# Kernel optimization log

Hardware: AMD Instinct MI355X
Metric: run time of the kernel (lower is better)

## Reference

```python
import jax, jax.numpy as jnp
import numpy as np

B, H, W, C = 8, 28, 28, 1024
NH = 16
HD = C // NH          # head dim 64
HID = 4 * C           # mlp hidden 4096
BC = C // 2           # bottleneck channels 512
SCALE = HD ** -0.5


def setup_inputs() -> dict:
    key = jax.random.key(0)
    ks = iter(jax.random.split(key, 32))
    def rn(shape, s=0.02):
        return jax.random.normal(next(ks), shape, jnp.float32) * s
    return dict(
        x=jax.random.normal(next(ks), (B, H, W, C), jnp.float32),
        norm1_w=jnp.ones((C,), jnp.float32), norm1_b=jnp.zeros((C,), jnp.float32),
        qkv_w=rn((C, 3 * C)), qkv_b=jnp.zeros((3 * C,), jnp.float32),
        proj_w=rn((C, C)), proj_b=jnp.zeros((C,), jnp.float32),
        rel_h=rn((2 * H - 1, HD)), rel_w=rn((2 * W - 1, HD)),
        norm2_w=jnp.ones((C,), jnp.float32), norm2_b=jnp.zeros((C,), jnp.float32),
        fc1_w=rn((C, HID)), fc1_b=jnp.zeros((HID,), jnp.float32),
        fc2_w=rn((HID, C)), fc2_b=jnp.zeros((C,), jnp.float32),
        conv1_w=rn((1, 1, C, BC)), ln1_w=jnp.ones((BC,), jnp.float32), ln1_b=jnp.zeros((BC,), jnp.float32),
        conv2_w=rn((3, 3, BC, BC)), ln2_w=jnp.ones((BC,), jnp.float32), ln2_b=jnp.zeros((BC,), jnp.float32),
        conv3_w=rn((1, 1, BC, C)), ln3_w=rn((C,)), ln3_b=rn((C,)),
    )


def _ln(x, w, b, eps):
    # layernorm over last axis (channels in NHWC)
    m = jnp.mean(x, -1, keepdims=True)
    v = jnp.mean((x - m) ** 2, -1, keepdims=True)
    return (x - m) * jax.lax.rsqrt(v + eps) * w + b


def _conv(x, w, pad):
    return jax.lax.conv_general_dilated(
        x, w, (1, 1), pad, dimension_numbers=('NHWC', 'HWIO', 'NHWC'))


def _gelu(x):
    return jax.nn.gelu(x, approximate=False)


def _block_forward(x, norm1_w, norm1_b, qkv_w, qkv_b, proj_w, proj_b,
                   rel_h, rel_w, norm2_w, norm2_b, fc1_w, fc1_b, fc2_w, fc2_b,
                   conv1_w, ln1_w, ln1_b, conv2_w, ln2_w, ln2_b, conv3_w, ln3_w, ln3_b):
    S = H * W
    shortcut = x
    xn = _ln(x, norm1_w, norm1_b, 1e-5)

    # ---- attention with decomposed relative position bias ----
    qkv = xn.reshape(B, S, C) @ qkv_w + qkv_b                 # [B,S,3C]
    qkv = qkv.reshape(B, S, 3, NH, HD).transpose(2, 0, 3, 1, 4)  # [3,B,nh,S,hd]
    q, k, v = qkv[0], qkv[1], qkv[2]
    attn = jnp.einsum('bnsd,bntd->bnst', q * SCALE, k)        # [B,nh,S,S]

    idx_h = jnp.arange(H)[:, None] - jnp.arange(H)[None, :] + (H - 1)
    idx_w = jnp.arange(W)[:, None] - jnp.arange(W)[None, :] + (W - 1)
    Rh = rel_h[idx_h]   # [H,H,hd]
    Rw = rel_w[idx_w]   # [W,W,hd]
    qr = q.reshape(B, NH, H, W, HD)
    bias_h = jnp.einsum('bnhwd,hkd->bnhwk', qr, Rh)           # [B,nh,H,W,H]
    bias_w = jnp.einsum('bnhwd,wkd->bnhwk', qr, Rw)           # [B,nh,H,W,W]
    attn = (attn.reshape(B, NH, H, W, H, W)
            + bias_h[..., :, None] + bias_w[..., None, :]).reshape(B, NH, S, S)

    attn = jax.nn.softmax(attn, axis=-1)
    out = jnp.einsum('bnst,bntd->bnsd', attn, v)              # [B,nh,S,hd]
    out = out.transpose(0, 2, 1, 3).reshape(B, H, W, C)
    out = out @ proj_w + proj_b

    x = shortcut + out

    # ---- MLP ----
    xn = _ln(x, norm2_w, norm2_b, 1e-5)
    x = x + (_gelu(xn.reshape(B, S, C) @ fc1_w + fc1_b) @ fc2_w + fc2_b).reshape(B, H, W, C)

    # ---- residual bottleneck conv (channel LayerNorm, eps=1e-6) ----
    out = _conv(x, conv1_w, 'VALID')
    out = _gelu(_ln(out, ln1_w, ln1_b, 1e-6))
    out = _conv(out, conv2_w, ((1, 1), (1, 1)))
    out = _gelu(_ln(out, ln2_w, ln2_b, 1e-6))
    out = _conv(out, conv3_w, 'VALID')
    out = _ln(out, ln3_w, ln3_b, 1e-6)
    return x + out


def reference(x, norm1_w, norm1_b, qkv_w, qkv_b, proj_w, proj_b,
              rel_h, rel_w, norm2_w, norm2_b, fc1_w, fc1_b, fc2_w, fc2_b,
              conv1_w, ln1_w, ln1_b, conv2_w, ln2_w, ln2_b, conv3_w, ln3_w, ln3_b):
    return _block_forward(x, norm1_w, norm1_b, qkv_w, qkv_b, proj_w, proj_b,
                          rel_h, rel_w, norm2_w, norm2_b, fc1_w, fc1_b, fc2_w, fc2_b,
                          conv1_w, ln1_w, ln1_b, conv2_w, ln2_w, ln2_b, conv3_w, ln3_w, ln3_b)
```

## Files before the change

kernel.cpp:

```cpp
#include <hip/hip_runtime.h>
#include <cstdint>
#include <cstddef>

using u16 = unsigned short;
using u32 = unsigned int;

__device__ __forceinline__ float bf2f(u16 u){
  union { u32 i; float f; } x; x.i = ((u32)u) << 16; return x.f;
}
__device__ __forceinline__ u16 f2bf(float f){
  union { float f; u32 i; } x; x.f = f;
  u32 r = x.i + 0x7fffu + ((x.i >> 16) & 1u);
  return (u16)(r >> 16);
}
__device__ __forceinline__ float gelu_f(float x){
  return 0.5f * x * (1.0f + erff(x * 0.70710678118654752f));
}
__device__ __forceinline__ void gld16(const void* g, void* l){
  __builtin_amdgcn_global_load_lds((__attribute__((address_space(1))) void*)(void*)g,
                                   (__attribute__((address_space(3))) void*)l, 16, 0, 0);
}

typedef __bf16 bf16x8 __attribute__((ext_vector_type(8)));
typedef float  f32x4  __attribute__((ext_vector_type(4)));

__global__ __launch_bounds__(256) void k_transpose(const float* __restrict__ src,
                                                   u16* __restrict__ dst, int R, int C){
  __shared__ u16 tile[32][33];
  int bx = blockIdx.x * 32;
  int by = blockIdx.y * 32;
  int tx = threadIdx.x & 31;
  int ty = threadIdx.x >> 5;
  for (int r = ty; r < 32; r += 8)
    tile[r][tx] = f2bf(src[(size_t)(by + r) * C + bx + tx]);
  __syncthreads();
  for (int r = ty; r < 32; r += 8)
    dst[(size_t)(bx + r) * R + by + tx] = tile[tx][r];
}

template<bool IN_F32, bool DO_GELU>
__global__ __launch_bounds__(256) void k_layernorm(const void* __restrict__ inp,
    const float* __restrict__ w, const float* __restrict__ bsh,
    u16* __restrict__ out, int cols, float eps){
  int row = blockIdx.x, t = threadIdx.x;
  size_t base = (size_t)row * cols;
  const float* inf = (const float*)inp;
  const u16*  inb = (const u16*)inp;
  float v[4];
  int ep = cols >> 8;
  float s = 0.f, ss = 0.f;
  for (int e = 0; e < ep; ++e){
    int idx = t + (e << 8);
    float x = IN_F32 ? inf[base + idx] : bf2f(inb[base + idx]);
    v[e] = x; s += x; ss += x * x;
  }
#pragma unroll
  for (int off = 1; off < 64; off <<= 1){
    s  += __shfl_xor(s, off, 64);
    ss += __shfl_xor(ss, off, 64);
  }
  __shared__ float red[8];
  int wv = t >> 6;
  if ((t & 63) == 0){ red[wv] = s; red[4 + wv] = ss; }
  __syncthreads();
  s  = red[0] + red[1] + red[2] + red[3];
  ss = red[4] + red[5] + red[6] + red[7];
  float inv = 1.f / (float)cols;
  float mean = s * inv;
  float var = ss * inv - mean * mean;
  float rs = rsqrtf(var + eps);
  for (int e = 0; e < ep; ++e){
    int idx = t + (e << 8);
    float y = (v[e] - mean) * rs * w[idx] + bsh[idx];
    if (DO_GELU) y = gelu_f(y);
    out[base + idx] = f2bf(y);
  }
}

__global__ __launch_bounds__(256) void k_final(const u16* __restrict__ c3,
    const u16* __restrict__ x2, const float* __restrict__ w,
    const float* __restrict__ bsh, float* __restrict__ out){
  int row = blockIdx.x, t = threadIdx.x;
  size_t base = (size_t)row << 10;
  float v[4];
  float s = 0.f, ss = 0.f;
#pragma unroll
  for (int e = 0; e < 4; ++e){
    int idx = t + (e << 8);
    float x = bf2f(c3[base + idx]);
    v[e] = x; s += x; ss += x * x;
  }
#pragma unroll
  for (int off = 1; off < 64; off <<= 1){
    s  += __shfl_xor(s, off, 64);
    ss += __shfl_xor(ss, off, 64);
  }
  __shared__ float red[8];
  int wv = t >> 6;
  if ((t & 63) == 0){ red[wv] = s; red[4 + wv] = ss; }
  __syncthreads();
  s  = red[0] + red[1] + red[2] + red[3];
  ss = red[4] + red[5] + red[6] + red[7];
  float mean = s * (1.f/1024.f);
  float var = ss * (1.f/1024.f) - mean * mean;
  float rs = rsqrtf(var + 1e-6f);
#pragma unroll
  for (int e = 0; e < 4; ++e){
    int idx = t + (e << 8);
    float y = (v[e] - mean) * rs * w[idx] + bsh[idx];
    out[base + idx] = bf2f(x2[base + idx]) + y;
  }
}

template<bool BIAS, bool GELU, bool RES, bool OUTB, bool OUTF>
__global__ __launch_bounds__(256, 2) void k_gemm(
    const u16* __restrict__ A, const u16* __restrict__ Bt,
    const float* __restrict__ bias, const float* __restrict__ resf,
    u16* __restrict__ outb, float* __restrict__ outf, int N, int K)
{
  __shared__ __align__(16) u16 As[128 * 32];
  __shared__ __align__(16) u16 Bs[128 * 32];
  int t = threadIdx.x, lane = t & 63, wv = t >> 6;
  int m0 = blockIdx.y << 7, n0 = blockIdx.x << 7;
  int wm = (wv >> 1) << 6, wn = (wv & 1) << 6;

  f32x4 acc[4][4];
  const f32x4 z4 = {0.f, 0.f, 0.f, 0.f};
#pragma unroll
  for (int i = 0; i < 4; ++i)
#pragma unroll
    for (int j = 0; j < 4; ++j) acc[i][j] = z4;

  int srow = (wv << 5) + (lane >> 2);
  int skp  = (lane & 3) << 3;
  const u16* Ag = A  + (size_t)(m0 + srow) * K + skp;
  const u16* Bg = Bt + (size_t)(n0 + srow) * K + skp;
  u16* As0 = &As[(wv << 5) * 32];
  u16* As1 = As0 + 16 * 32;
  u16* Bs0 = &Bs[(wv << 5) * 32];
  u16* Bs1 = Bs0 + 16 * 32;
  const size_t rowskip = (size_t)16 * K;

  int fr = lane & 15, fq = (lane >> 4) << 3;

  for (int k0 = 0; k0 < K; k0 += 32){
    gld16(Ag + k0, As0);
    gld16(Ag + rowskip + k0, As1);
    gld16(Bg + k0, Bs0);
    gld16(Bg + rowskip + k0, Bs1);
    __syncthreads();
    bf16x8 af[4], bfr[4];
#pragma unroll
    for (int i = 0; i < 4; ++i)
      af[i] = *(const bf16x8*)&As[(wm + i * 16 + fr) * 32 + fq];
#pragma unroll
    for (int j = 0; j < 4; ++j)
      bfr[j] = *(const bf16x8*)&Bs[(wn + j * 16 + fr) * 32 + fq];
#pragma unroll
    for (int i = 0; i < 4; ++i)
#pragma unroll
      for (int j = 0; j < 4; ++j)
        acc[i][j] = __builtin_amdgcn_mfma_f32_16x16x32_bf16(af[i], bfr[j], acc[i][j], 0, 0, 0);
    __syncthreads();
  }

  int rr = (lane >> 4) << 2;
  int cc = lane & 15;
#pragma unroll
  for (int i = 0; i < 4; ++i)
#pragma unroll
    for (int j = 0; j < 4; ++j){
      int gc = n0 + wn + j * 16 + cc;
      float bb = BIAS ? bias[gc] : 0.f;
#pragma unroll
      for (int r = 0; r < 4; ++r){
        int gr = m0 + wm + i * 16 + rr + r;
        size_t idx = (size_t)gr * N + gc;
        float vv = acc[i][j][r] + bb;
        if (RES) vv += resf[idx];
        if (GELU) vv = gelu_f(vv);
        if (OUTF) outf[idx] = vv;
        if (OUTB) outb[idx] = f2bf(vv);
      }
    }
}

#define ATT_STR 72
__global__ __launch_bounds__(256, 3) void k_attn3(const u16* __restrict__ qkv,
    const float* __restrict__ relh, const float* __restrict__ relw,
    u16* __restrict__ out)
{
  __shared__ __align__(16) u16 k_s[64 * ATT_STR];
  __shared__ __align__(16) u16 vT_s[80 * ATT_STR];
  __shared__ __align__(16) u16 p_s[128 * ATT_STR];
  __shared__ u16 gh_s[128 * 28];
  __shared__ u16 gw_s[128 * 28];

  const int t = threadIdx.x, lane = t & 63, wv = t >> 6;
  int id = blockIdx.x;
  int xr = id & 7, rest = id >> 3;
  int qt = rest % 7, gg = rest / 7;
  int bnh = xr + (gg << 3);
  const int b = bnh >> 4, nh = bnh & 15;
  const int q0 = qt << 7;
  const size_t rowbase = (size_t)b * 784;
  const int wq0 = wv << 5;
  const int fr = lane & 15;
  const int fq = lane >> 4;

  u16* rh_s = p_s;
  u16* rw_s = p_s + 64 * ATT_STR;
  {
    int row = t >> 2, c0 = (t & 3) << 4;
    u16 bh_[16], bw_[16];
    if (row < 55){
      const float* ph = relh + row * 64 + c0;
      const float* pw = relw + row * 64 + c0;
#pragma unroll
      for (int e = 0; e < 16; ++e){ bh_[e] = f2bf(ph[e]); bw_[e] = f2bf(pw[e]); }
    } else {
#pragma unroll
      for (int e = 0; e < 16; ++e){ bh_[e] = 0; bw_[e] = 0; }
    }
    *(uint4*)&rh_s[row * ATT_STR + c0]     = *(uint4*)bh_;
    *(uint4*)&rh_s[row * ATT_STR + c0 + 8] = *(uint4*)(bh_ + 8);
    *(uint4*)&rw_s[row * ATT_STR + c0]     = *(uint4*)bw_;
    *(uint4*)&rw_s[row * ATT_STR + c0 + 8] = *(uint4*)(bw_ + 8);
    for (int idx = t; idx < 16 * ATT_STR; idx += 256){
      int rr = idx / ATT_STR, cc = idx - rr * ATT_STR;
      vT_s[(64 + rr) * ATT_STR + cc] = (rr == 0 && cc < 64) ? (u16)0x3f80 : (u16)0;
    }
  }

  bf16x8 qf[2][2];
#pragma unroll
  for (int mf = 0; mf < 2; ++mf)
#pragma unroll
    for (int ks = 0; ks < 2; ++ks){
      int row = q0 + wq0 + mf * 16 + fr;
      if (row < 784){
        qf[mf][ks] = *(const bf16x8*)(qkv + (rowbase + row) * 3072 + nh * 64 + fq * 8 + ks * 32);
      } else {
        uint4 z = {0u,0u,0u,0u}; qf[mf][ks] = *(bf16x8*)&z;
      }
    }
  __syncthreads();

  const f32x4 z4 = {0.f,0.f,0.f,0.f};
#pragma unroll
  for (int which = 0; which < 2; ++which){
    const u16* rs = which ? rw_s : rh_s;
    f32x4 G[2][4];
#pragma unroll
    for (int mf = 0; mf < 2; ++mf)
#pragma unroll
      for (int nf = 0; nf < 4; ++nf) G[mf][nf] = z4;
#pragma unroll
    for (int nf = 0; nf < 4; ++nf){
      bf16x8 rf0 = *(const bf16x8*)&rs[(nf * 16 + fr) * ATT_STR + fq * 8];
      bf16x8 rf1 = *(const bf16x8*)&rs[(nf * 16 + fr) * ATT_STR + fq * 8 + 32];
#pragma unroll
      for (int mf = 0; mf < 2; ++mf){
        G[mf][nf] = __builtin_amdgcn_mfma_f32_16x16x32_bf16(qf[mf][0], rf0, G[mf][nf], 0, 0, 0);
        G[mf][nf] = __builtin_amdgcn_mfma_f32_16x16x32_bf16(qf[mf][1], rf1, G[mf][nf], 0, 0, 0);
      }
    }
    u16* gt = which ? gw_s : gh_s;
#pragma unroll
    for (int mf = 0; mf < 2; ++mf)
#pragma unroll
      for (int r = 0; r < 4; ++r){
        int lr = wq0 + mf * 16 + fq * 4 + r;
        int grow = q0 + lr;
        int hq = grow / 28;
        int coord = which ? (grow - hq * 28) : hq;
#pragma unroll
        for (int nf = 0; nf < 4; ++nf){
          int j = nf * 16 + fr;
          int kk = coord + 27 - j;
          if ((unsigned)kk < 28u) gt[lr * 28 + kk] = f2bf(G[mf][nf][r]);
        }
      }
  }
  __syncthreads();

  f32x4 acc[2][5];
#pragma unroll
  for (int mf = 0; mf < 2; ++mf)
#pragma unroll
    for (int nf = 0; nf < 5; ++nf) acc[mf][nf] = z4;

  for (int kt = 0; kt < 13; ++kt){
    __syncthreads();
    {
      int krow = lane;
      int d0 = wv << 4;
      int jg = (kt << 6) + krow;
      uint4 kv0 = {0u,0u,0u,0u}, kv1 = {0u,0u,0u,0u};
      uint4 vv0 = {0u,0u,0u,0u}, vv1 = {0u,0u,0u,0u};
      if (jg < 784){
        const u16* kp = qkv + (rowbase + jg) * 3072 + 1024 + nh * 64 + d0;
        kv0 = *(const uint4*)kp; kv1 = *(const uint4*)(kp + 8);
        vv0 = *(const uint4*)(kp + 1024); vv1 = *(const uint4*)(kp + 1032);
      }
      *(uint4*)&k_s[krow * ATT_STR + d0]     = kv0;
      *(uint4*)&k_s[krow * ATT_STR + d0 + 8] = kv1;
      u16 vbuf[16];
      *(uint4*)vbuf = vv0; *(uint4*)(vbuf + 8) = vv1;
#pragma unroll
      for (int e = 0; e < 16; ++e) vT_s[(d0 + e) * ATT_STR + krow] = vbuf[e];
    }
    __syncthreads();

    f32x4 S[2][4];
#pragma unroll
    for (int nf = 0; nf < 4; ++nf){
      bf16x8 kf0 = *(const bf16x8*)&k_s[(nf * 16 + fr) * ATT_STR + fq * 8];
      bf16x8 kf1 = *(const bf16x8*)&k_s[(nf * 16 + fr) * ATT_STR + fq * 8 + 32];
#pragma unroll
      for (int mf = 0; mf < 2; ++mf){
        f32x4 s = z4;
        s = __builtin_amdgcn_mfma_f32_16x16x32_bf16(qf[mf][0], kf0, s, 0, 0, 0);
        s = __builtin_amdgcn_mfma_f32_16x16x32_bf16(qf[mf][1], kf1, s, 0, 0, 0);
        S[mf][nf] = s;
      }
    }

    int hj[4], wj[4]; bool val[4];
#pragma unroll
    for (int nf = 0; nf < 4; ++nf){
      int jg = (kt << 6) + nf * 16 + fr;
      int h = jg / 28;
      hj[nf] = h; wj[nf] = jg - h * 28; val[nf] = (jg < 784);
    }
#pragma unroll
    for (int mf = 0; mf < 2; ++mf)
#pragma unroll
      for (int r = 0; r < 4; ++r){
        int lr = wq0 + mf * 16 + fq * 4 + r;
#pragma unroll
        for (int nf = 0; nf < 4; ++nf){
          float p = 0.f;
          if (val[nf]){
            float bias = bf2f(gh_s[lr * 28 + hj[nf]]) + bf2f(gw_s[lr * 28 + wj[nf]]);
            p = __expf(fmaf(0.125f, S[mf][nf][r], bias));
          }
          p_s[lr * ATT_STR + nf * 16 + fr] = f2bf(p);
        }
      }

#pragma unroll
    for (int ks = 0; ks < 2; ++ks){
      bf16x8 pf0 = *(const bf16x8*)&p_s[(wq0 + fr) * ATT_STR + fq * 8 + ks * 32];
      bf16x8 pf1 = *(const bf16x8*)&p_s[(wq0 + 16 + fr) * ATT_STR + fq * 8 + ks * 32];
#pragma unroll
      for (int nf = 0; nf < 5; ++nf){
        bf16x8 vf = *(const bf16x8*)&vT_s[(nf * 16 + fr) * ATT_STR + fq * 8 + ks * 32];
        acc[0][nf] = __builtin_amdgcn_mfma_f32_16x16x32_bf16(pf0, vf, acc[0][nf], 0, 0, 0);
        acc[1][nf] = __builtin_amdgcn_mfma_f32_16x16x32_bf16(pf1, vf, acc[1][nf], 0, 0, 0);
      }
    }
  }

#pragma unroll
  for (int mf = 0; mf < 2; ++mf)
#pragma unroll
    for (int r = 0; r < 4; ++r){
      float l = __shfl(acc[mf][4][r], lane & 48, 64);
      int row = q0 + wq0 + mf * 16 + fq * 4 + r;
      if (row < 784){
        float inv = 1.f / l;
        u16* dp = out + (rowbase + row) * 1024 + nh * 64 + fr;
#pragma unroll
        for (int nf = 0; nf < 4; ++nf)
          dp[nf * 16] = f2bf(acc[mf][nf][r] * inv);
      }
    }
}

__global__ __launch_bounds__(256) void k_im2col(const u16* __restrict__ g, u16* __restrict__ im){
  int idx = blockIdx.x * 256 + threadIdx.x;
  int p  = idx / 576;
  int c8 = idx - p * 576;
  int k0 = c8 << 3;
  int t9 = k0 >> 9;
  int ci = k0 & 511;
  int ky = t9 / 3, kx = t9 - ky * 3;
  int bb = p / 784;
  int s = p - bb * 784;
  int h = s / 28, w = s - h * 28;
  int hh = h + ky - 1, ww = w + kx - 1;
  uint4 val = make_uint4(0u, 0u, 0u, 0u);
  if ((unsigned)hh < 28u && (unsigned)ww < 28u)
    val = *(const uint4*)&g[(((size_t)(bb * 28 + hh)) * 28 + ww) * 512 + ci];
  *(uint4*)&im[(size_t)p * 4608 + k0] = val;
}

extern "C" void kernel_launch(void* const* d_in, const int* in_sizes, int n_in,
                              void* d_out, int out_size, void* d_ws, size_t ws_size,
                              hipStream_t stream)
{
  (void)in_sizes; (void)n_in; (void)out_size; (void)ws_size;
  const float* x      = (const float*)d_in[0];
  const float* n1w    = (const float*)d_in[1];
  const float* n1b    = (const float*)d_in[2];
  const float* qkv_w  = (const float*)d_in[3];
  const float* qkv_b  = (const float*)d_in[4];
  const float* proj_w = (const float*)d_in[5];
  const float* proj_b = (const float*)d_in[6];
  const float* rel_h  = (const float*)d_in[7];
  const float* rel_w  = (const float*)d_in[8];
  const float* n2w    = (const float*)d_in[9];
  const float* n2b    = (const float*)d_in[10];
  const float* fc1_w  = (const float*)d_in[11];
  const float* fc1_b  = (const float*)d_in[12];
  const float* fc2_w  = (const float*)d_in[13];
  const float* fc2_b  = (const float*)d_in[14];
  const float* c1w    = (const float*)d_in[15];
  const float* l1w    = (const float*)d_in[16];
  const float* l1b    = (const float*)d_in[17];
  const float* c2w    = (const float*)d_in[18];
  const float* l2w    = (const float*)d_in[19];
  const float* l2b    = (const float*)d_in[20];
  const float* c3w    = (const float*)d_in[21];
  const float* l3w    = (const float*)d_in[22];
  const float* l3b    = (const float*)d_in[23];

  char* ws = (char*)d_ws;
  size_t off = 0;
  auto alloc = [&](size_t bytes) -> void* {
    void* p = ws + off; off += (bytes + 255) & ~(size_t)255; return p;
  };
  const size_t M = 6272;
  u16* qkvT  = (u16*)alloc((size_t)3072 * 1024 * 2);
  u16* projT = (u16*)alloc((size_t)1024 * 1024 * 2);
  u16* fc1T  = (u16*)alloc((size_t)4096 * 1024 * 2);
  u16* fc2T  = (u16*)alloc((size_t)1024 * 4096 * 2);
  u16* c1T   = (u16*)alloc((size_t)512 * 1024 * 2);
  u16* c2T   = (u16*)alloc((size_t)512 * 4608 * 2);
  u16* c3T   = (u16*)alloc((size_t)1024 * 512 * 2);
  u16* qkvbuf = (u16*)alloc(M * 3072 * 2);
  u16* attn   = (u16*)alloc(M * 1024 * 2);
  u16* xn     = (u16*)alloc(M * 1024 * 2);
  float* x1   = (float*)alloc(M * 1024 * 4);
  u16* x2b    = (u16*)alloc(M * 1024 * 2);
  u16* c1buf  = (u16*)alloc(M * 512 * 2);
  u16* g1buf  = (u16*)alloc(M * 512 * 2);
  u16* hmlp   = qkvbuf;
  u16* im     = qkvbuf;
  u16* xn2    = xn;
  u16* c2buf  = c1buf;
  u16* g2buf  = g1buf;
  u16* c3buf  = attn;

  dim3 blk(256);
  k_transpose<<<dim3(3072/32, 1024/32), blk, 0, stream>>>(qkv_w, qkvT, 1024, 3072);
  k_transpose<<<dim3(1024/32, 1024/32), blk, 0, stream>>>(proj_w, projT, 1024, 1024);
  k_transpose<<<dim3(4096/32, 1024/32), blk, 0, stream>>>(fc1_w, fc1T, 1024, 4096);
  k_transpose<<<dim3(1024/32, 4096/32), blk, 0, stream>>>(fc2_w, fc2T, 4096, 1024);
  k_transpose<<<dim3(512/32, 1024/32),  blk, 0, stream>>>(c1w, c1T, 1024, 512);
  k_transpose<<<dim3(512/32, 4608/32),  blk, 0, stream>>>(c2w, c2T, 4608, 512);
  k_transpose<<<dim3(1024/32, 512/32),  blk, 0, stream>>>(c3w, c3T, 512, 1024);

  k_layernorm<true,false><<<6272, blk, 0, stream>>>(x, n1w, n1b, xn, 1024, 1e-5f);
  k_gemm<true,false,false,true,false><<<dim3(24,49), blk, 0, stream>>>(
      xn, qkvT, qkv_b, nullptr, qkvbuf, nullptr, 3072, 1024);
  k_attn3<<<896, blk, 0, stream>>>(qkvbuf, rel_h, rel_w, attn);
  k_gemm<true,false,true,false,true><<<dim3(8,49), blk, 0, stream>>>(
      attn, projT, proj_b, x, nullptr, x1, 1024, 1024);
  k_layernorm<true,false><<<6272, blk, 0, stream>>>(x1, n2w, n2b, xn2, 1024, 1e-5f);
  k_gemm<true,true,false,true,false><<<dim3(32,49), blk, 0, stream>>>(
      xn2, fc1T, fc1_b, nullptr, hmlp, nullptr, 4096, 1024);
  k_gemm<true,false,true,true,false><<<dim3(8,49), blk, 0, stream>>>(
      hmlp, fc2T, fc2_b, x1, x2b, nullptr, 1024, 4096);
  k_gemm<false,false,false,true,false><<<dim3(4,49), blk, 0, stream>>>(
      x2b, c1T, nullptr, nullptr, c1buf, nullptr, 512, 1024);
  k_layernorm<false,true><<<6272, blk, 0, stream>>>(c1buf, l1w, l1b, g1buf, 512, 1e-6f);
  k_im2col<<<14112, blk, 0, stream>>>(g1buf, im);
  k_gemm<false,false,false,true,false><<<dim3(4,49), blk, 0, stream>>>(
      im, c2T, nullptr, nullptr, c2buf, nullptr, 512, 4608);
  k_layernorm<false,true><<<6272, blk, 0, stream>>>(c2buf, l2w, l2b, g2buf, 512, 1e-6f);
  k_gemm<false,false,false,true,false><<<dim3(8,49), blk, 0, stream>>>(
      g2buf, c3T, nullptr, nullptr, c3buf, nullptr, 1024, 512);
  k_final<<<6272, blk, 0, stream>>>(c3buf, x2b, l3w, l3b, (float*)d_out);
}
```

Measured before the change: 743.6 us.

## Merge weight transposes into one launch and rework attention score layout

Combines the seven per-weight transpose launches into a single kernel that reads a packed descriptor table, which cuts launch overhead. The attention kernel now pre-scales q by 1/8 and the relative-position tables by 8. It computes S transposed (K as the A operand) so each lane holds four consecutive keys, and writes packed bias-plus-exp results. It also XOR-swizzles K in LDS, writes V transposed as paired 32-bit stores, and pads the width-bias table to a stride of 31 to cut bank conflicts. The GEMM occupancy hint rises from 2 to 3 blocks per CU, which may force register spills.

Measured after the change: 744.1 us. Within noise of the previous version (+0.1%).

```diff
diff --git a/kernel.cpp b/kernel.cpp
--- a/kernel.cpp
+++ b/kernel.cpp
@@ -24,11 +24,22 @@
 typedef __bf16 bf16x8 __attribute__((ext_vector_type(8)));
 typedef float  f32x4  __attribute__((ext_vector_type(4)));
 
-__global__ __launch_bounds__(256) void k_transpose(const float* __restrict__ src,
-                                                   u16* __restrict__ dst, int R, int C){
+struct TransPack {
+  const float* src[7]; u16* dst[7];
+  int R[7], C[7], base[8];
+};
+__global__ __launch_bounds__(256) void k_transpose_all(TransPack p){
   __shared__ u16 tile[32][33];
-  int bx = blockIdx.x * 32;
-  int by = blockIdx.y * 32;
+  int bid = blockIdx.x;
+  int m = 0;
+#pragma unroll
+  for (int i = 1; i < 7; ++i) if (bid >= p.base[i]) m = i;
+  int local = bid - p.base[m];
+  const float* src = p.src[m]; u16* dst = p.dst[m];
+  int R = p.R[m], C = p.C[m];
+  int tilesx = C >> 5;
+  int bx = (local % tilesx) << 5;
+  int by = (local / tilesx) << 5;
   int tx = threadIdx.x & 31;
   int ty = threadIdx.x >> 5;
   for (int r = ty; r < 32; r += 8)
@@ -113,7 +124,7 @@
 }
 
 template<bool BIAS, bool GELU, bool RES, bool OUTB, bool OUTF>
-__global__ __launch_bounds__(256, 2) void k_gemm(
+__global__ __launch_bounds__(256, 3) void k_gemm(
     const u16* __restrict__ A, const u16* __restrict__ Bt,
     const float* __restrict__ bias, const float* __restrict__ resf,
     u16* __restrict__ outb, float* __restrict__ outf, int N, int K)
@@ -186,7 +197,7 @@
 }
 
 #define ATT_STR 72
-__global__ __launch_bounds__(256, 3) void k_attn3(const u16* __restrict__ qkv,
+__global__ __launch_bounds__(256, 3) void k_attn4(const u16* __restrict__ qkv,
     const float* __restrict__ relh, const float* __restrict__ relw,
     u16* __restrict__ out)
 {
@@ -194,7 +205,7 @@
   __shared__ __align__(16) u16 vT_s[80 * ATT_STR];
   __shared__ __align__(16) u16 p_s[128 * ATT_STR];
   __shared__ u16 gh_s[128 * 28];
-  __shared__ u16 gw_s[128 * 28];
+  __shared__ u16 gw_s[128 * 31];
 
   const int t = threadIdx.x, lane = t & 63, wv = t >> 6;
   int id = blockIdx.x;
@@ -217,7 +228,7 @@
       const float* ph = relh + row * 64 + c0;
       const float* pw = relw + row * 64 + c0;
 #pragma unroll
-      for (int e = 0; e < 16; ++e){ bh_[e] = f2bf(ph[e]); bw_[e] = f2bf(pw[e]); }
+      for (int e = 0; e < 16; ++e){ bh_[e] = f2bf(ph[e] * 8.f); bw_[e] = f2bf(pw[e] * 8.f); }
     } else {
 #pragma unroll
       for (int e = 0; e < 16; ++e){ bh_[e] = 0; bw_[e] = 0; }
@@ -238,11 +249,18 @@
 #pragma unroll
     for (int ks = 0; ks < 2; ++ks){
       int row = q0 + wq0 + mf * 16 + fr;
+      u16 qs[8];
       if (row < 784){
-        qf[mf][ks] = *(const bf16x8*)(qkv + (rowbase + row) * 3072 + nh * 64 + fq * 8 + ks * 32);
+        const u16* qp = qkv + (rowbase + row) * 3072 + nh * 64 + fq * 8 + ks * 32;
+        uint4 q4 = *(const uint4*)qp;
+        u16 qe[8]; *(uint4*)qe = q4;
+#pragma unroll
+        for (int e = 0; e < 8; ++e) qs[e] = f2bf(bf2f(qe[e]) * 0.125f);
       } else {
-        uint4 z = {0u,0u,0u,0u}; qf[mf][ks] = *(bf16x8*)&z;
-      }
+#pragma unroll
+        for (int e = 0; e < 8; ++e) qs[e] = 0;
+      }
+      qf[mf][ks] = *(bf16x8*)qs;
     }
   __syncthreads();
 
@@ -266,6 +284,7 @@
       }
     }
     u16* gt = which ? gw_s : gh_s;
+    int GSTR = which ? 31 : 28;
 #pragma unroll
     for (int mf = 0; mf < 2; ++mf)
 #pragma unroll
@@ -278,11 +297,15 @@
         for (int nf = 0; nf < 4; ++nf){
           int j = nf * 16 + fr;
           int kk = coord + 27 - j;
-          if ((unsigned)kk < 28u) gt[lr * 28 + kk] = f2bf(G[mf][nf][r]);
+          if ((unsigned)kk < 28u) gt[lr * GSTR + kk] = f2bf(G[mf][nf][r]);
         }
       }
   }
   __syncthreads();
+  for (int idx = t; idx < 128 * 3; idx += 256){
+    int q = idx / 3, i = idx - q * 3;
+    gw_s[q * 31 + 28 + i] = gw_s[q * 31 + i];
+  }
 
   f32x4 acc[2][5];
 #pragma unroll
@@ -297,57 +320,71 @@
       int d0 = wv << 4;
       int jg = (kt << 6) + krow;
       uint4 kv0 = {0u,0u,0u,0u}, kv1 = {0u,0u,0u,0u};
-      uint4 vv0 = {0u,0u,0u,0u}, vv1 = {0u,0u,0u,0u};
       if (jg < 784){
         const u16* kp = qkv + (rowbase + jg) * 3072 + 1024 + nh * 64 + d0;
         kv0 = *(const uint4*)kp; kv1 = *(const uint4*)(kp + 8);
-        vv0 = *(const uint4*)(kp + 1024); vv1 = *(const uint4*)(kp + 1032);
-      }
-      *(uint4*)&k_s[krow * ATT_STR + d0]     = kv0;
-      *(uint4*)&k_s[krow * ATT_STR + d0 + 8] = kv1;
-      u16 vbuf[16];
-      *(uint4*)vbuf = vv0; *(uint4*)(vbuf + 8) = vv1;
-#pragma unroll
-      for (int e = 0; e < 16; ++e) vT_s[(d0 + e) * ATT_STR + krow] = vbuf[e];
+      }
+      int g = (krow >> 3) & 7;
+      int c0 = wv << 1;
+      *(uint4*)&k_s[krow * ATT_STR + ((c0 ^ g) << 3)]       = kv0;
+      *(uint4*)&k_s[krow * ATT_STR + (((c0 + 1) ^ g) << 3)] = kv1;
+      int j2 = t & 31, dgrp = t >> 5;
+      int d0v = dgrp << 3;
+      int ja = (kt << 6) + (j2 << 1), jb = ja + 1;
+      uint4 va = {0u,0u,0u,0u}, vb = {0u,0u,0u,0u};
+      if (ja < 784) va = *(const uint4*)(qkv + (rowbase + ja) * 3072 + 2048 + nh * 64 + d0v);
+      if (jb < 784) vb = *(const uint4*)(qkv + (rowbase + jb) * 3072 + 2048 + nh * 64 + d0v);
+      u16 va_[8], vb_[8];
+      *(uint4*)va_ = va; *(uint4*)vb_ = vb;
+#pragma unroll
+      for (int e = 0; e < 8; ++e)
+        *(u32*)&vT_s[(d0v + e) * ATT_STR + (j2 << 1)] = (u32)va_[e] | ((u32)vb_[e] << 16);
     }
     __syncthreads();
 
-    f32x4 S[2][4];
-#pragma unroll
-    for (int nf = 0; nf < 4; ++nf){
-      bf16x8 kf0 = *(const bf16x8*)&k_s[(nf * 16 + fr) * ATT_STR + fq * 8];
-      bf16x8 kf1 = *(const bf16x8*)&k_s[(nf * 16 + fr) * ATT_STR + fq * 8 + 32];
+    f32x4 S[4][2];
+#pragma unroll
+    for (int kf = 0; kf < 4; ++kf){
+      int row = kf * 16 + fr;
+      int g = (row >> 3) & 7;
+      bf16x8 kA0 = *(const bf16x8*)&k_s[row * ATT_STR + ((fq ^ g) << 3)];
+      bf16x8 kA1 = *(const bf16x8*)&k_s[row * ATT_STR + (((fq + 4) ^ g) << 3)];
 #pragma unroll
       for (int mf = 0; mf < 2; ++mf){
         f32x4 s = z4;
-        s = __builtin_amdgcn_mfma_f32_16x16x32_bf16(qf[mf][0], kf0, s, 0, 0, 0);
-        s = __builtin_amdgcn_mfma_f32_16x16x32_bf16(qf[mf][1], kf1, s, 0, 0, 0);
-        S[mf][nf] = s;
-      }
-    }
-
-    int hj[4], wj[4]; bool val[4];
-#pragma unroll
-    for (int nf = 0; nf < 4; ++nf){
-      int jg = (kt << 6) + nf * 16 + fr;
-      int h = jg / 28;
-      hj[nf] = h; wj[nf] = jg - h * 28; val[nf] = (jg < 784);
-    }
-#pragma unroll
-    for (int mf = 0; mf < 2; ++mf)
-#pragma unroll
-      for (int r = 0; r < 4; ++r){
-        int lr = wq0 + mf * 16 + fq * 4 + r;
-#pragma unroll
-        for (int nf = 0; nf < 4; ++nf){
-          float p = 0.f;
-          if (val[nf]){
-            float bias = bf2f(gh_s[lr * 28 + hj[nf]]) + bf2f(gw_s[lr * 28 + wj[nf]]);
-            p = __expf(fmaf(0.125f, S[mf][nf][r], bias));
-          }
-          p_s[lr * ATT_STR + nf * 16 + fr] = f2bf(p);
+        s = __builtin_amdgcn_mfma_f32_16x16x32_bf16(kA0, qf[mf][0], s, 0, 0, 0);
+        s = __builtin_amdgcn_mfma_f32_16x16x32_bf16(kA1, qf[mf][1], s, 0, 0, 0);
+        S[kf][mf] = s;
+      }
+    }
+
+#pragma unroll
+    for (int mf = 0; mf < 2; ++mf){
+      int qrl = wq0 + mf * 16 + fr;
+      const u16* ghrow = &gh_s[qrl * 28];
+      const u16* gwrow = &gw_s[qrl * 31];
+#pragma unroll
+      for (int kf = 0; kf < 4; ++kf){
+        int j0 = (kt << 6) + kf * 16 + (fq << 2);
+        int j0c = min(j0, 783), j3c = min(j0 + 3, 783);
+        int h0 = j0c / 28, h3 = j3c / 28;
+        int w0 = j0c - h0 * 28;
+        float gh0 = bf2f(ghrow[h0]), gh3 = bf2f(ghrow[h3]);
+        float p[4];
+#pragma unroll
+        for (int r = 0; r < 4; ++r){
+          int w = w0 + r;
+          float ghv = (w >= 28) ? gh3 : gh0;
+          float gwv = bf2f(gwrow[w]);
+          float sc = S[kf][mf][r] + ghv + gwv;
+          p[r] = (j0 + r < 784) ? __expf(sc) : 0.f;
         }
-      }
+        u32 lo = (u32)f2bf(p[0]) | ((u32)f2bf(p[1]) << 16);
+        u32 hi = (u32)f2bf(p[2]) | ((u32)f2bf(p[3]) << 16);
+        uint2 pk; pk.x = lo; pk.y = hi;
+        *(uint2*)&p_s[qrl * ATT_STR + kf * 16 + (fq << 2)] = pk;
+      }
+    }
 
 #pragma unroll
     for (int ks = 0; ks < 2; ++ks){
@@ -363,7 +400,7 @@
   }
 
 #pragma unroll
-  for (int mf = 0; mf < 2; ++mf)
+  for (int mf = 0; mf < 2; ++mf){
 #pragma unroll
     for (int r = 0; r < 4; ++r){
       float l = __shfl(acc[mf][4][r], lane & 48, 64);
@@ -376,6 +413,7 @@
           dp[nf * 16] = f2bf(acc[mf][nf][r] * inv);
       }
     }
+  }
 }
 
 __global__ __launch_bounds__(256) void k_im2col(const u16* __restrict__ g, u16* __restrict__ im){
@@ -454,18 +492,26 @@
   u16* c3buf  = attn;
 
   dim3 blk(256);
-  k_transpose<<<dim3(3072/32, 1024/32), blk, 0, stream>>>(qkv_w, qkvT, 1024, 3072);
-  k_transpose<<<dim3(1024/32, 1024/32), blk, 0, stream>>>(proj_w, projT, 1024, 1024);
-  k_transpose<<<dim3(4096/32, 1024/32), blk, 0, stream>>>(fc1_w, fc1T, 1024, 4096);
-  k_transpose<<<dim3(1024/32, 4096/32), blk, 0, stream>>>(fc2_w, fc2T, 4096, 1024);
-  k_transpose<<<dim3(512/32, 1024/32),  blk, 0, stream>>>(c1w, c1T, 1024, 512);
-  k_transpose<<<dim3(512/32, 4608/32),  blk, 0, stream>>>(c2w, c2T, 4608, 512);
-  k_transpose<<<dim3(1024/32, 512/32),  blk, 0, stream>>>(c3w, c3T, 512, 1024);
+  {
+    TransPack tp;
+    const float* srcs[7] = {qkv_w, proj_w, fc1_w, fc2_w, c1w, c2w, c3w};
+    u16* dsts[7] = {qkvT, projT, fc1T, fc2T, c1T, c2T, c3T};
+    int Rs[7] = {1024, 1024, 1024, 4096, 1024, 4608, 512};
+    int Cs[7] = {3072, 1024, 4096, 1024, 512, 512, 1024};
+    int base = 0;
+    for (int i = 0; i < 7; ++i){
+      tp.src[i] = srcs[i]; tp.dst[i] = dsts[i]; tp.R[i] = Rs[i]; tp.C[i] = Cs[i];
+      tp.base[i] = base;
+      base += (Rs[i] >> 5) * (Cs[i] >> 5);
+    }
+    tp.base[7] = base;
+    k_transpose_all<<<base, blk, 0, stream>>>(tp);
+  }
 
   k_layernorm<true,false><<<6272, blk, 0, stream>>>(x, n1w, n1b, xn, 1024, 1e-5f);
   k_gemm<true,false,false,true,false><<<dim3(24,49), blk, 0, stream>>>(
       xn, qkvT, qkv_b, nullptr, qkvbuf, nullptr, 3072, 1024);
-  k_attn3<<<896, blk, 0, stream>>>(qkvbuf, rel_h, rel_w, attn);
+  k_attn4<<<896, blk, 0, stream>>>(qkvbuf, rel_h, rel_w, attn);
   k_gemm<true,false,true,false,true><<<dim3(8,49), blk, 0, stream>>>(
       attn, projT, proj_b, x, nullptr, x1, 1024, 1024);
   k_layernorm<true,false><<<6272, blk, 0, stream>>>(x1, n2w, n2b, xn2, 1024, 1e-5f);
```
